# Performance work log

Hardware: AMD Instinct MI355X
Metric: run time of the kernel (lower is better)

The kernel has to match this reference:

```python
import jax, jax.numpy as jnp
import numpy as np

TEMPERATURE = 0.5
EPS = 1e-10

N, C, H, W = 8, 256, 96, 96
T, V = 32, 256
NUM_CLASSES = 19


def setup_inputs() -> dict:
    key = jax.random.key(0)
    k1, k2, k3, k4 = jax.random.split(key, 4)
    features = jax.random.normal(k1, (N, C, H, W), dtype=jnp.float32)
    batch_inds = jax.random.randint(k2, (T,), 0, N, dtype=jnp.int32)
    sample_inds = jax.random.randint(k3, (T, V), 0, H * W).astype(jnp.int64)
    labels = jax.random.randint(k4, (T,), 0, NUM_CLASSES, dtype=jnp.int32)
    return {"features": features, "batch_inds": batch_inds,
            "sample_inds": sample_inds, "labels": labels}


def reference(features, batch_inds, sample_inds, labels):
    n, c, h, w = features.shape
    t, v = sample_inds.shape
    # --- anchor sampling: gather V pixels per (image, class) pair ---
    f = features.reshape(n, c, h * w)            # (N, C, HW)
    g = f[batch_inds]                            # (T, C, HW)
    sampled = jnp.take_along_axis(g, sample_inds[:, None, :], axis=2)  # (T, C, V)
    # --- contrastive loss ---
    norm = jnp.maximum(jnp.linalg.norm(sampled, axis=1, keepdims=True), 1e-12)
    feats = sampled / norm                       # L2 normalize along C
    feats = jnp.swapaxes(feats, 1, 2).reshape(t * v, c)  # (T*V, C)
    lab = jnp.repeat(labels, v)                  # (T*V,)
    dot = (feats @ feats.T) / TEMPERATURE        # (T*V, T*V)
    eq = (lab[:, None] == lab[None, :]).astype(dot.dtype)
    diag = jnp.eye(t * v, dtype=dot.dtype)
    pos_mask = eq * (1.0 - diag)
    neg_mask = 1.0 - eq
    # stable SupCon loss: logsumexp over {self-exp + all negatives}
    logits = dot - jax.lax.stop_gradient(jnp.max(dot, axis=1, keepdims=True))
    exp_logits = jnp.exp(logits)
    neg_sum = jnp.sum(exp_logits * neg_mask, axis=1, keepdims=True)
    log_prob = logits - jnp.log(exp_logits + neg_sum)
    mean_log_prob_pos = jnp.sum(pos_mask * log_prob, axis=1) / jnp.maximum(
        jnp.sum(pos_mask, axis=1), EPS)
    return -jnp.mean(mean_log_prob_pos)
```

## Files before the change

### kernel.cpp

```cpp
#include <hip/hip_runtime.h>
#include <hip/hip_bf16.h>


namespace {

constexpr int kC = 256;
constexpr int kHW = 96 * 96;
constexpr int kT = 32;
constexpr int kV = 256;
constexpr int kM = kT * kV;

typedef __attribute__((ext_vector_type(8))) short short8;
typedef __attribute__((ext_vector_type(4))) float f32x4;

__device__ inline unsigned short f2bf(float x) {
  __hip_bfloat16 h = __float2bfloat16(x);
  return __builtin_bit_cast(unsigned short, h);
}
__device__ inline float bf2f(unsigned short u) {
  unsigned int v = ((unsigned int)u) << 16;
  return __builtin_bit_cast(float, v);
}
__device__ inline void load_lds16(const unsigned short* g, unsigned short* l) {
  __builtin_amdgcn_global_load_lds(
      (const __attribute__((address_space(1))) void*)g,
      (__attribute__((address_space(3))) void*)l, 16, 0, 0);
}

__device__ inline void stage_tile(const unsigned short* __restrict__ F,
                                  unsigned short* lds, int ct, int w,
                                  int lane) {
#pragma unroll
  for (int i = 0; i < 8; ++i) {
    const int n = w * 512 + i * 64 + lane;
    const int j = n >> 5;
    const int m = (lane & 31) ^ (j & 31);
    load_lds16(F + ((size_t)(ct * 64 + j) << 8) + m * 8,
               lds + (size_t)(w * 512 + i * 64) * 8);
  }
}

}

__global__ __launch_bounds__(256) void k_gather(
    const float* __restrict__ feat, const int* __restrict__ binds,
    const int* __restrict__ sinds, unsigned short* __restrict__ FT) {
  const int b = (int)blockIdx.x;
  const int c = (int)blockIdx.y;
  __shared__ alignas(16) float row[kHW];
  __shared__ int s_match[kT + 1];
  if (threadIdx.x == 0) {
    int cnt = 0;
    for (int t = 0; t < kT; ++t)
      if (binds[t] == b) s_match[1 + cnt++] = t;
    s_match[0] = cnt;
  }
  __syncthreads();
  const int cnt = s_match[0];
  if (cnt == 0) return;
  const float4* src4 = (const float4*)(feat + ((size_t)b * kC + c) * kHW);
  for (int i = (int)threadIdx.x; i < kHW / 4; i += 256)
    ((float4*)row)[i] = src4[i];
  __syncthreads();
  unsigned short* dst = FT + (size_t)c * kM;
  for (int mi = 1; mi <= cnt; ++mi) {
    const int t = s_match[mi];
    const int p = sinds[t * kV + threadIdx.x];
    dst[t * kV + threadIdx.x] = f2bf(row[p]);
  }
}

__global__ __launch_bounds__(256) void k_norm(
    const unsigned short* __restrict__ FT, unsigned short* __restrict__ F) {
  constexpr int PAD = 40;
  const int v0 = (int)blockIdx.x * 32;
  __shared__ alignas(16) unsigned short tile[kC][PAD];
  __shared__ float part[8][32];
  __shared__ float s_inv[32];
  const int tid = (int)threadIdx.x;
  {
    const int p4 = tid & 3, cb = tid >> 2;
    for (int c = cb; c < kC; c += 64) {
      int4 d = *(const int4*)(FT + (size_t)c * kM + v0 + p4 * 8);
      *(int4*)&tile[c][p4 * 8] = d;
    }
  }
  __syncthreads();
  {
    const int v = tid & 31, oct = tid >> 5;
    float ss = 0.f;
    for (int c = oct * 32; c < oct * 32 + 32; ++c) {
      float x = bf2f(tile[c][v]);
      ss += x * x;
    }
    part[oct][v] = ss;
  }
  __syncthreads();
  if (tid < 32) {
    float ss = 0.f;
#pragma unroll
    for (int o = 0; o < 8; ++o) ss += part[o][tid];
    s_inv[tid] = 1.0f / fmaxf(sqrtf(ss), 1e-12f);
  }
  __syncthreads();
#pragma unroll
  for (int p = 0; p < 4; ++p) {
    const int chunk = p * 256 + tid;
    const int v = chunk >> 5, c0 = (chunk & 31) << 3;
    const float inv = s_inv[v];
    alignas(16) unsigned short o[8];
#pragma unroll
    for (int k = 0; k < 8; ++k) o[k] = f2bf(bf2f(tile[c0 + k][v]) * inv);
    *(int4*)(F + (size_t)(v0 + v) * kC + c0) = *(const int4*)o;
  }
}

__global__ __launch_bounds__(256, 2) void k_neg(
    const unsigned short* __restrict__ F, const int* __restrict__ labels,
    float* __restrict__ ns) {
  const int tid = (int)threadIdx.x;
  const int w = tid >> 6, lane = tid & 63, q = lane >> 4, l16 = lane & 15;
  const int bid = (int)blockIdx.x;
  const int xcd = bid & 7, slot = bid >> 3;
  const int cx = xcd >> 1;
  const int row0 = (((slot << 1) | (xcd & 1))) * 64;
  __shared__ alignas(16) unsigned short Bt[2][64 * kC];
  __shared__ int s_lab[kT];
  __shared__ int s_tiles[32];
  __shared__ int s_nt;
  __shared__ float s_red[4][64];
  if (tid < kT) s_lab[tid] = labels[tid];
  __syncthreads();
  const int labr = s_lab[row0 >> 8];
  if (tid == 0) {
    int n = 0;
    for (int ct = cx * 32; ct < cx * 32 + 32; ++ct)
      if (s_lab[ct >> 2] != labr) s_tiles[n++] = ct;
    s_nt = n;
  }
  __syncthreads();
  const int nt = s_nt;
  if (nt == 0) return;

  short8 af[4][8];
#pragma unroll
  for (int rg = 0; rg < 4; ++rg)
#pragma unroll
    for (int ks = 0; ks < 8; ++ks)
      af[rg][ks] = *(const short8*)((const short*)F +
                                    (size_t)(row0 + rg * 16 + l16) * kC +
                                    ks * 32 + q * 8);

  const int j2 = w * 16 + l16;
  int bofs[8];
#pragma unroll
  for (int ks = 0; ks < 8; ++ks)
    bofs[ks] = ((ks * 4 + q) ^ (j2 & 31)) << 3;

  stage_tile(F, Bt[0], s_tiles[0], w, lane);
  __syncthreads();

  float sacc[4][4] = {};
  int cur = 0;
  for (int it = 0; it < nt; ++it) {
    if (it + 1 < nt) stage_tile(F, Bt[cur ^ 1], s_tiles[it + 1], w, lane);
    const unsigned short* bcol = Bt[cur] + j2 * kC;
    f32x4 acc[4];
#pragma unroll
    for (int rg = 0; rg < 4; ++rg) acc[rg] = (f32x4){0.f, 0.f, 0.f, 0.f};
#pragma unroll
    for (int ks = 0; ks < 8; ++ks) {
      short8 bf = *(const short8*)(bcol + bofs[ks]);
#pragma unroll
      for (int rg = 0; rg < 4; ++rg)
        acc[rg] = __builtin_amdgcn_mfma_f32_16x16x32_bf16(af[rg][ks], bf,
                                                          acc[rg], 0, 0, 0);
    }
#pragma unroll
    for (int rg = 0; rg < 4; ++rg)
#pragma unroll
      for (int r = 0; r < 4; ++r)
        sacc[rg][r] += __expf(fmaf(acc[rg][r], 2.f, -2.f));
    __syncthreads();
    cur ^= 1;
  }
#pragma unroll
  for (int rg = 0; rg < 4; ++rg)
#pragma unroll
    for (int r = 0; r < 4; ++r) {
      float v = sacc[rg][r];
      v += __shfl_xor(v, 1, 64);
      v += __shfl_xor(v, 2, 64);
      v += __shfl_xor(v, 4, 64);
      v += __shfl_xor(v, 8, 64);
      if (l16 == 0) s_red[w][rg * 16 + q * 4 + r] = v;
    }
  __syncthreads();
  if (tid < 64) {
    float v = s_red[0][tid] + s_red[1][tid] + s_red[2][tid] + s_red[3][tid];
    atomicAdd(&ns[row0 + tid], v);
  }
}

__global__ __launch_bounds__(256, 2) void k_pos(
    const unsigned short* __restrict__ F, const int* __restrict__ labels,
    const float* __restrict__ ns, float* __restrict__ out) {
  const int tid = (int)threadIdx.x;
  const int w = tid >> 6, lane = tid & 63, q = lane >> 4, l16 = lane & 15;
  const int row0 = (int)blockIdx.y * 64;
  const int tcol = (int)blockIdx.x;
  __shared__ alignas(16) unsigned short Bt[2][64 * kC];
  __shared__ int s_lab[kT];
  __shared__ float s_pos[4];
  if (tid < kT) s_lab[tid] = labels[tid];
  __syncthreads();
  const int labr = s_lab[row0 >> 8];
  if (s_lab[tcol] != labr) return;

  short8 af[4][8];
#pragma unroll
  for (int rg = 0; rg < 4; ++rg)
#pragma unroll
    for (int ks = 0; ks < 8; ++ks)
      af[rg][ks] = *(const short8*)((const short*)F +
                                    (size_t)(row0 + rg * 16 + l16) * kC +
                                    ks * 32 + q * 8);
  const int j2 = w * 16 + l16;
  int bofs[8];
#pragma unroll
  for (int ks = 0; ks < 8; ++ks)
    bofs[ks] = ((ks * 4 + q) ^ (j2 & 31)) << 3;

  float nsv[4][4];
#pragma unroll
  for (int rg = 0; rg < 4; ++rg)
#pragma unroll
    for (int r = 0; r < 4; ++r)
      nsv[rg][r] = ns[row0 + rg * 16 + q * 4 + r];

  stage_tile(F, Bt[0], tcol * 4, w, lane);
  __syncthreads();

  float pos = 0.f;
  int cur = 0;
  for (int ti = 0; ti < 4; ++ti) {
    const int ct = tcol * 4 + ti;
    if (ti < 3) stage_tile(F, Bt[cur ^ 1], ct + 1, w, lane);
    const unsigned short* bcol = Bt[cur] + j2 * kC;
    f32x4 acc[4];
#pragma unroll
    for (int rg = 0; rg < 4; ++rg) acc[rg] = (f32x4){0.f, 0.f, 0.f, 0.f};
#pragma unroll
    for (int ks = 0; ks < 8; ++ks) {
      short8 bf = *(const short8*)(bcol + bofs[ks]);
#pragma unroll
      for (int rg = 0; rg < 4; ++rg)
        acc[rg] = __builtin_amdgcn_mfma_f32_16x16x32_bf16(af[rg][ks], bf,
                                                          acc[rg], 0, 0, 0);
    }
    const int jcol = ct * 64 + j2;
#pragma unroll
    for (int rg = 0; rg < 4; ++rg)
#pragma unroll
      for (int r = 0; r < 4; ++r) {
        const int i = row0 + rg * 16 + q * 4 + r;
        if (i != jcol) {
          float d = fmaf(acc[rg][r], 2.f, -2.f);
          pos += d - __logf(__expf(d) + nsv[rg][r]);
        }
      }
    __syncthreads();
    cur ^= 1;
  }
#pragma unroll
  for (int m = 1; m < 64; m <<= 1) pos += __shfl_xor(pos, m, 64);
  if (lane == 0) s_pos[w] = pos;
  __syncthreads();
  if (tid == 0) {
    float tot = s_pos[0] + s_pos[1] + s_pos[2] + s_pos[3];
    int matches = 0;
    for (int t = 0; t < kT; ++t) matches += (s_lab[t] == labr) ? 1 : 0;
    const float cnt = (float)(matches * kV - 1);
    atomicAdd(out, -tot / (cnt * (float)kM));
  }
}

extern "C" void kernel_launch(void* const* d_in, const int* in_sizes, int n_in,
                              void* d_out, int out_size, void* d_ws,
                              size_t ws_size, hipStream_t stream) {
  const float* feat = (const float*)d_in[0];
  const int* binds = (const int*)d_in[1];
  const int* sinds = (const int*)d_in[2];
  const int* labels = (const int*)d_in[3];
  float* out = (float*)d_out;
  unsigned short* FT = (unsigned short*)d_ws;
  unsigned short* F = FT + (size_t)kC * kM;
  float* ns = (float*)(F + (size_t)kM * kC);

  hipMemsetAsync(d_out, 0, sizeof(float) * out_size, stream);
  hipMemsetAsync(ns, 0, sizeof(float) * kM, stream);
  k_gather<<<dim3(8, kC), 256, 0, stream>>>(feat, binds, sinds, FT);
  k_norm<<<kM / 32, 256, 0, stream>>>(FT, F);
  k_neg<<<dim3(512), 256, 0, stream>>>(F, labels, ns);
  k_pos<<<dim3(kT, kM / 64), 256, 0, stream>>>(F, labels, ns, out);
}
```

Before: 201.4 us.

## Fold memsets into k_norm, retile k_neg to 2x2 waves, split k_pos grid

Removes the two hipMemsetAsync launches by zeroing ns and out inside block 0 of k_norm. k_neg now stages its row tile in LDS and lays the four waves out as a 2x2 grid, each computing 32x32 instead of 64x16. This halves A-fragment registers and raises B reuse per LDS read. k_pos goes from a 32x128 grid with four sequential column tiles per block to a 128x128 grid with one tile per block, which trades pipelining for more parallelism.

```diff
diff --git a/kernel.cpp b/kernel.cpp
--- a/kernel.cpp
+++ b/kernel.cpp
@@ -71,13 +71,18 @@
 }
 
 __global__ __launch_bounds__(256) void k_norm(
-    const unsigned short* __restrict__ FT, unsigned short* __restrict__ F) {
+    const unsigned short* __restrict__ FT, unsigned short* __restrict__ F,
+    float* __restrict__ ns, float* __restrict__ out, int out_size) {
   constexpr int PAD = 40;
   const int v0 = (int)blockIdx.x * 32;
   __shared__ alignas(16) unsigned short tile[kC][PAD];
   __shared__ float part[8][32];
   __shared__ float s_inv[32];
   const int tid = (int)threadIdx.x;
+  if (blockIdx.x == 0) {
+    for (int i = tid; i < kM; i += 256) ns[i] = 0.f;
+    for (int i = tid; i < out_size; i += 256) out[i] = 0.f;
+  }
   {
     const int p4 = tid & 3, cb = tid >> 2;
     for (int c = cb; c < kC; c += 64) {
@@ -120,6 +125,7 @@
     float* __restrict__ ns) {
   const int tid = (int)threadIdx.x;
   const int w = tid >> 6, lane = tid & 63, q = lane >> 4, l16 = lane & 15;
+  const int wr = w >> 1, wc = w & 1;
   const int bid = (int)blockIdx.x;
   const int xcd = bid & 7, slot = bid >> 3;
   const int cx = xcd >> 1;
@@ -128,7 +134,7 @@
   __shared__ int s_lab[kT];
   __shared__ int s_tiles[32];
   __shared__ int s_nt;
-  __shared__ float s_red[4][64];
+  __shared__ float s_red[4][32];
   if (tid < kT) s_lab[tid] = labels[tid];
   __syncthreads();
   const int labr = s_lab[row0 >> 8];
@@ -142,50 +148,59 @@
   const int nt = s_nt;
   if (nt == 0) return;
 
-  short8 af[4][8];
-#pragma unroll
-  for (int rg = 0; rg < 4; ++rg)
+  stage_tile(F, Bt[0], row0 >> 6, w, lane);
+  stage_tile(F, Bt[1], s_tiles[0], w, lane);
+  __syncthreads();
+
+  short8 af[2][8];
+#pragma unroll
+  for (int rg = 0; rg < 2; ++rg) {
+    const int ja = wr * 32 + rg * 16 + l16;
+    const unsigned short* arow = Bt[0] + ja * kC;
 #pragma unroll
     for (int ks = 0; ks < 8; ++ks)
-      af[rg][ks] = *(const short8*)((const short*)F +
-                                    (size_t)(row0 + rg * 16 + l16) * kC +
-                                    ks * 32 + q * 8);
-
-  const int j2 = w * 16 + l16;
-  int bofs[8];
-#pragma unroll
-  for (int ks = 0; ks < 8; ++ks)
-    bofs[ks] = ((ks * 4 + q) ^ (j2 & 31)) << 3;
-
-  stage_tile(F, Bt[0], s_tiles[0], w, lane);
-  __syncthreads();
-
-  float sacc[4][4] = {};
-  int cur = 0;
+      af[rg][ks] = *(const short8*)(arow + (((ks * 4 + q) ^ (ja & 31)) << 3));
+  }
+  __syncthreads();
+
+  const int jb0 = wc * 32 + l16, jb1 = wc * 32 + 16 + l16;
+  const unsigned short* bc0base = (const unsigned short*)Bt + jb0 * kC;
+  const unsigned short* bc1base = (const unsigned short*)Bt + jb1 * kC;
+  int bofs0[8], bofs1[8];
+#pragma unroll
+  for (int ks = 0; ks < 8; ++ks) {
+    bofs0[ks] = (((ks * 4 + q) ^ (jb0 & 31)) << 3);
+    bofs1[ks] = (((ks * 4 + q) ^ (jb1 & 31)) << 3);
+  }
+
+  float sacc[2][4] = {};
   for (int it = 0; it < nt; ++it) {
-    if (it + 1 < nt) stage_tile(F, Bt[cur ^ 1], s_tiles[it + 1], w, lane);
-    const unsigned short* bcol = Bt[cur] + j2 * kC;
-    f32x4 acc[4];
-#pragma unroll
-    for (int rg = 0; rg < 4; ++rg) acc[rg] = (f32x4){0.f, 0.f, 0.f, 0.f};
+    if (it + 1 < nt) stage_tile(F, Bt[it & 1], s_tiles[it + 1], w, lane);
+    const size_t boff = (size_t)(1 ^ (it & 1)) * (64 * kC);
+    const unsigned short* bc0 = bc0base + boff;
+    const unsigned short* bc1 = bc1base + boff;
+    f32x4 a00 = {0.f, 0.f, 0.f, 0.f}, a01 = a00, a10 = a00, a11 = a00;
 #pragma unroll
     for (int ks = 0; ks < 8; ++ks) {
-      short8 bf = *(const short8*)(bcol + bofs[ks]);
-#pragma unroll
-      for (int rg = 0; rg < 4; ++rg)
-        acc[rg] = __builtin_amdgcn_mfma_f32_16x16x32_bf16(af[rg][ks], bf,
-                                                          acc[rg], 0, 0, 0);
-    }
-#pragma unroll
-    for (int rg = 0; rg < 4; ++rg)
-#pragma unroll
-      for (int r = 0; r < 4; ++r)
-        sacc[rg][r] += __expf(fmaf(acc[rg][r], 2.f, -2.f));
+      short8 b0 = *(const short8*)(bc0 + bofs0[ks]);
+      short8 b1 = *(const short8*)(bc1 + bofs1[ks]);
+      a00 = __builtin_amdgcn_mfma_f32_16x16x32_bf16(af[0][ks], b0, a00, 0, 0, 0);
+      a01 = __builtin_amdgcn_mfma_f32_16x16x32_bf16(af[0][ks], b1, a01, 0, 0, 0);
+      a10 = __builtin_amdgcn_mfma_f32_16x16x32_bf16(af[1][ks], b0, a10, 0, 0, 0);
+      a11 = __builtin_amdgcn_mfma_f32_16x16x32_bf16(af[1][ks], b1, a11, 0, 0, 0);
+    }
+#pragma unroll
+    for (int r = 0; r < 4; ++r) {
+      sacc[0][r] += __expf(fmaf(a00[r], 2.f, -2.f)) +
+                    __expf(fmaf(a01[r], 2.f, -2.f));
+      sacc[1][r] += __expf(fmaf(a10[r], 2.f, -2.f)) +
+                    __expf(fmaf(a11[r], 2.f, -2.f));
+    }
     __syncthreads();
-    cur ^= 1;
-  }
-#pragma unroll
-  for (int rg = 0; rg < 4; ++rg)
+  }
+
+#pragma unroll
+  for (int rg = 0; rg < 2; ++rg)
 #pragma unroll
     for (int r = 0; r < 4; ++r) {
       float v = sacc[rg][r];
@@ -197,7 +212,8 @@
     }
   __syncthreads();
   if (tid < 64) {
-    float v = s_red[0][tid] + s_red[1][tid] + s_red[2][tid] + s_red[3][tid];
+    const int rr = tid >> 5, e = tid & 31;
+    float v = s_red[rr * 2][e] + s_red[rr * 2 + 1][e];
     atomicAdd(&ns[row0 + tid], v);
   }
 }
@@ -207,15 +223,18 @@
     const float* __restrict__ ns, float* __restrict__ out) {
   const int tid = (int)threadIdx.x;
   const int w = tid >> 6, lane = tid & 63, q = lane >> 4, l16 = lane & 15;
-  const int row0 = (int)blockIdx.y * 64;
-  const int tcol = (int)blockIdx.x;
-  __shared__ alignas(16) unsigned short Bt[2][64 * kC];
+  const int bi = (int)blockIdx.y;
+  const int bj = (int)blockIdx.x;
+  __shared__ alignas(16) unsigned short Bt[64 * kC];
   __shared__ int s_lab[kT];
   __shared__ float s_pos[4];
   if (tid < kT) s_lab[tid] = labels[tid];
   __syncthreads();
-  const int labr = s_lab[row0 >> 8];
-  if (s_lab[tcol] != labr) return;
+  const int labr = s_lab[bi >> 2];
+  if (s_lab[bj >> 2] != labr) return;
+  const int row0 = bi * 64;
+
+  stage_tile(F, Bt, bj, w, lane);
 
   short8 af[4][8];
 #pragma unroll
@@ -226,6 +245,7 @@
                                     (size_t)(row0 + rg * 16 + l16) * kC +
                                     ks * 32 + q * 8);
   const int j2 = w * 16 + l16;
+  const unsigned short* bcol = Bt + j2 * kC;
   int bofs[8];
 #pragma unroll
   for (int ks = 0; ks < 8; ++ks)
@@ -238,40 +258,31 @@
     for (int r = 0; r < 4; ++r)
       nsv[rg][r] = ns[row0 + rg * 16 + q * 4 + r];
 
-  stage_tile(F, Bt[0], tcol * 4, w, lane);
-  __syncthreads();
-
+  __syncthreads();
+
+  f32x4 acc[4];
+#pragma unroll
+  for (int rg = 0; rg < 4; ++rg) acc[rg] = (f32x4){0.f, 0.f, 0.f, 0.f};
+#pragma unroll
+  for (int ks = 0; ks < 8; ++ks) {
+    short8 bf = *(const short8*)(bcol + bofs[ks]);
+#pragma unroll
+    for (int rg = 0; rg < 4; ++rg)
+      acc[rg] = __builtin_amdgcn_mfma_f32_16x16x32_bf16(af[rg][ks], bf,
+                                                        acc[rg], 0, 0, 0);
+  }
+  const int jcol = bj * 64 + j2;
   float pos = 0.f;
-  int cur = 0;
-  for (int ti = 0; ti < 4; ++ti) {
-    const int ct = tcol * 4 + ti;
-    if (ti < 3) stage_tile(F, Bt[cur ^ 1], ct + 1, w, lane);
-    const unsigned short* bcol = Bt[cur] + j2 * kC;
-    f32x4 acc[4];
-#pragma unroll
-    for (int rg = 0; rg < 4; ++rg) acc[rg] = (f32x4){0.f, 0.f, 0.f, 0.f};
-#pragma unroll
-    for (int ks = 0; ks < 8; ++ks) {
-      short8 bf = *(const short8*)(bcol + bofs[ks]);
-#pragma unroll
-      for (int rg = 0; rg < 4; ++rg)
-        acc[rg] = __builtin_amdgcn_mfma_f32_16x16x32_bf16(af[rg][ks], bf,
-                                                          acc[rg], 0, 0, 0);
-    }
-    const int jcol = ct * 64 + j2;
-#pragma unroll
-    for (int rg = 0; rg < 4; ++rg)
-#pragma unroll
-      for (int r = 0; r < 4; ++r) {
-        const int i = row0 + rg * 16 + q * 4 + r;
-        if (i != jcol) {
-          float d = fmaf(acc[rg][r], 2.f, -2.f);
-          pos += d - __logf(__expf(d) + nsv[rg][r]);
-        }
+#pragma unroll
+  for (int rg = 0; rg < 4; ++rg)
+#pragma unroll
+    for (int r = 0; r < 4; ++r) {
+      const int i = row0 + rg * 16 + q * 4 + r;
+      if (i != jcol) {
+        float d = fmaf(acc[rg][r], 2.f, -2.f);
+        pos += d - __logf(__expf(d) + nsv[rg][r]);
       }
-    __syncthreads();
-    cur ^= 1;
-  }
+    }
 #pragma unroll
   for (int m = 1; m < 64; m <<= 1) pos += __shfl_xor(pos, m, 64);
   if (lane == 0) s_pos[w] = pos;
@@ -297,10 +308,8 @@
   unsigned short* F = FT + (size_t)kC * kM;
   float* ns = (float*)(F + (size_t)kM * kC);
 
-  hipMemsetAsync(d_out, 0, sizeof(float) * out_size, stream);
-  hipMemsetAsync(ns, 0, sizeof(float) * kM, stream);
   k_gather<<<dim3(8, kC), 256, 0, stream>>>(feat, binds, sinds, FT);
-  k_norm<<<kM / 32, 256, 0, stream>>>(FT, F);
+  k_norm<<<kM / 32, 256, 0, stream>>>(FT, F, ns, out, out_size);
   k_neg<<<dim3(512), 256, 0, stream>>>(F, labels, ns);
-  k_pos<<<dim3(kT, kM / 64), 256, 0, stream>>>(F, labels, ns, out);
-}
+  k_pos<<<dim3(128, 128), 256, 0, stream>>>(F, labels, ns, out);
+}
```

After: 212.7 us. +5.6%, slower.
